# Kernel tuning notes

Hardware: AMD Instinct MI355X
Metric: run time of the kernel (lower is better)

Reference implementation:

```python
import jax, jax.numpy as jnp
import numpy as np

RADIUS = 0.5
HEADS = 4
LATENT = 128
KIN = 3 + 3 + 3 + 1  # q_pos + o_pos + rel + dist
LN_EPS = 1e-5


def setup_inputs() -> dict:
    key = jax.random.key(0)
    ks = jax.random.split(key, 12)
    B, Nq, No = 2, 1024, 1024
    h_obs = jax.random.normal(ks[0], (B, No, LATENT), dtype=jnp.float32)
    pos_obs = jax.random.uniform(ks[1], (B, No, 3), dtype=jnp.float32)
    pos_query = jax.random.uniform(ks[2], (B, Nq, 3), dtype=jnp.float32)
    obs_mask = jax.random.randint(ks[3], (B, No), 0, 2, dtype=jnp.int32)
    # kernel MLP params: Linear(KIN, LATENT) -> ReLU -> Linear(LATENT, HEADS)
    W1 = jax.random.normal(ks[4], (KIN, LATENT), dtype=jnp.float32) * (1.0 / np.sqrt(KIN))
    b1 = jax.random.normal(ks[5], (LATENT,), dtype=jnp.float32) * 0.01
    W2 = jax.random.normal(ks[6], (LATENT, HEADS), dtype=jnp.float32) * (1.0 / np.sqrt(LATENT))
    b2 = jax.random.normal(ks[7], (HEADS,), dtype=jnp.float32) * 0.01
    ln_g = jnp.ones((LATENT,), dtype=jnp.float32)
    ln_b = jnp.zeros((LATENT,), dtype=jnp.float32)
    Wv = jax.random.normal(ks[8], (LATENT, LATENT), dtype=jnp.float32) * (1.0 / np.sqrt(LATENT))
    bv = jax.random.normal(ks[9], (LATENT,), dtype=jnp.float32) * 0.01
    return {"h_obs": h_obs, "pos_obs": pos_obs, "pos_query": pos_query,
            "obs_mask": obs_mask, "W1": W1, "b1": b1, "W2": W2, "b2": b2,
            "ln_g": ln_g, "ln_b": ln_b, "Wv": Wv, "bv": bv}


def reference(h_obs, pos_obs, pos_query, obs_mask, W1, b1, W2, b2, ln_g, ln_b, Wv, bv):
    B, Nq, _ = pos_query.shape
    _, No, _ = pos_obs.shape
    H, D = HEADS, LATENT // HEADS

    # pairwise geometric encoding: (B, Nq, No, *)
    rel = pos_query[:, :, None, :] - pos_obs[:, None, :, :]
    dist = jnp.linalg.norm(rel, axis=-1, keepdims=True)
    q_exp = jnp.broadcast_to(pos_query[:, :, None, :], rel.shape)
    o_exp = jnp.broadcast_to(pos_obs[:, None, :, :], rel.shape)
    kin = jnp.concatenate([q_exp, o_exp, rel, dist], axis=-1)  # (B,Nq,No,KIN)

    # per-pair MLP -> per-head attention logits
    hid = jax.nn.relu(kin @ W1 + b1)                 # (B,Nq,No,LATENT)
    logits = hid @ W2 + b2                           # (B,Nq,No,H)
    logits = jnp.transpose(logits, (0, 3, 1, 2))     # (B,H,Nq,No)

    # radius + observation masking
    neg = jnp.float32(-jnp.inf)
    mask = (dist[..., 0] > RADIUS)[:, None, :, :] | (obs_mask == 0)[:, None, None, :]
    logits = jnp.where(mask, neg, logits)
    weights = jax.nn.softmax(logits, axis=-1)        # (B,H,Nq,No)

    # value path: LayerNorm + projection
    mu = jnp.mean(h_obs, axis=-1, keepdims=True)
    var = jnp.var(h_obs, axis=-1, keepdims=True)
    hn = (h_obs - mu) / jnp.sqrt(var + LN_EPS) * ln_g + ln_b
    v = hn @ Wv + bv                                 # (B,No,LATENT)
    v = jnp.transpose(v.reshape(B, No, H, D), (0, 2, 1, 3))  # (B,H,No,D)

    out = jnp.einsum('bhqo,bhod->bhqd', weights, v)  # (B,H,Nq,D)
    out = jnp.transpose(out, (0, 2, 1, 3)).reshape(B, Nq, H * D)
    return out
```

## Files before the change

### kernel.cpp

```cpp
#include <hip/hip_runtime.h>
#include <math.h>
#include <float.h>

#define B_ 2
#define NQ 1024
#define NO 1024
#define LAT 128
#define NHEADS 4
#define RADIUS_ 0.5f
#define LN_EPS_ 1e-5f
#define CAP 256
#define PPAD 264

#define V_BYTES ((size_t)B_ * NO * LAT * 4)

__device__ __forceinline__ float selh(int h, float a, float b, float c, float d) {
  return h == 0 ? a : (h == 1 ? b : (h == 2 ? c : d));
}


__global__ __launch_bounds__(256) void gano_prep_kernel(
    const float* __restrict__ h_obs, const float* __restrict__ ln_g,
    const float* __restrict__ ln_b, const float* __restrict__ Wv,
    const float* __restrict__ bv, const float* __restrict__ W1,
    const float* __restrict__ b1, const float* __restrict__ W2,
    float* __restrict__ v_out,
    float4* __restrict__ A4, float4* __restrict__ CW8, int write_derived)
{
  const int tid = threadIdx.x;
  const int j = tid & 127;
  const int half = tid >> 7;
  const int wave = tid >> 6;
  const int lane = tid & 63;
  const int r0 = blockIdx.x * 4 + half * 2;

  __shared__ float s_redA[2][4];
  __shared__ float s_redB[2][4];
  __shared__ __align__(16) float s_hn[4][LAT];

  const float x0 = h_obs[(size_t)r0 * LAT + j];
  const float x1 = h_obs[(size_t)(r0 + 1) * LAT + j];
  float s0 = x0, s1 = x1;
  #pragma unroll
  for (int off = 32; off >= 1; off >>= 1) {
    s0 += __shfl_down(s0, off);
    s1 += __shfl_down(s1, off);
  }
  if (lane == 0) { s_redA[0][wave] = s0; s_redA[1][wave] = s1; }
  __syncthreads();
  const float mu0 = (s_redA[0][half * 2] + s_redA[0][half * 2 + 1]) * (1.0f / LAT);
  const float mu1 = (s_redA[1][half * 2] + s_redA[1][half * 2 + 1]) * (1.0f / LAT);
  const float d0 = x0 - mu0, d1 = x1 - mu1;
  float q0 = d0 * d0, q1 = d1 * d1;
  #pragma unroll
  for (int off = 32; off >= 1; off >>= 1) {
    q0 += __shfl_down(q0, off);
    q1 += __shfl_down(q1, off);
  }
  if (lane == 0) { s_redB[0][wave] = q0; s_redB[1][wave] = q1; }
  __syncthreads();
  const float var0 = (s_redB[0][half * 2] + s_redB[0][half * 2 + 1]) * (1.0f / LAT);
  const float var1 = (s_redB[1][half * 2] + s_redB[1][half * 2 + 1]) * (1.0f / LAT);
  const float g = ln_g[j], be = ln_b[j];
  s_hn[half * 2 + 0][j] = d0 * rsqrtf(var0 + LN_EPS_) * g + be;
  s_hn[half * 2 + 1][j] = d1 * rsqrtf(var1 + LN_EPS_) * g + be;
  __syncthreads();

  float a0 = 0.0f, a1 = 0.0f;
  const float4* h0 = (const float4*)s_hn[half * 2 + 0];
  const float4* h1 = (const float4*)s_hn[half * 2 + 1];
  #pragma unroll 4
  for (int k4 = 0; k4 < LAT / 4; ++k4) {
    const float4 u0 = h0[k4];
    const float4 u1 = h1[k4];
    const float w0 = Wv[(k4 * 4 + 0) * LAT + j];
    const float w1 = Wv[(k4 * 4 + 1) * LAT + j];
    const float w2 = Wv[(k4 * 4 + 2) * LAT + j];
    const float w3 = Wv[(k4 * 4 + 3) * LAT + j];
    a0 = fmaf(u0.x, w0, a0); a0 = fmaf(u0.y, w1, a0);
    a0 = fmaf(u0.z, w2, a0); a0 = fmaf(u0.w, w3, a0);
    a1 = fmaf(u1.x, w0, a1); a1 = fmaf(u1.y, w1, a1);
    a1 = fmaf(u1.z, w2, a1); a1 = fmaf(u1.w, w3, a1);
  }
  const float bvj = bv[j];
  v_out[(size_t)(r0 + 0) * LAT + j] = a0 + bvj;
  v_out[(size_t)(r0 + 1) * LAT + j] = a1 + bvj;

  if (write_derived && blockIdx.x == 0 && tid < LAT) {
    float w[10];
    #pragma unroll
    for (int k = 0; k < 10; ++k) w[k] = W1[k * LAT + tid];
    A4[tid] = make_float4(w[0] + w[6], w[1] + w[7], w[2] + w[8], b1[tid]);
    CW8[2 * tid + 0] = make_float4(w[3] - w[6], w[4] - w[7], w[5] - w[8], w[9]);
    CW8[2 * tid + 1] = make_float4(W2[tid * NHEADS + 0], W2[tid * NHEADS + 1],
                                   W2[tid * NHEADS + 2], W2[tid * NHEADS + 3]);
  }
}

template <int NS, bool DERIVED>
__device__ __forceinline__ void flash_pass(
    int lane, int cnt,
    const float4* __restrict__ s_list_w, const int* __restrict__ s_idx_w,
    const float* __restrict__ s_Qw, float* __restrict__ s_pw,
    const float4* __restrict__ CW8,
    const float* __restrict__ W1, const float* __restrict__ W2,
    float b20, float b21, float b22, float b23,
    const float* __restrict__ vb, int hh,
    float& m0, float& m1, float& m2, float& m3,
    float& z0, float& z1, float& z2, float& z3,
    float& ax, float& ay)
{
  float4 C[NS];
  bool act[NS];
  #pragma unroll
  for (int r = 0; r < NS; ++r) {
    const int s = r * 64 + lane;
    act[r] = s < cnt;
    C[r] = s_list_w[act[r] ? s : (cnt - 1)];
  }
  float L[NS][NHEADS];
  #pragma unroll
  for (int r = 0; r < NS; ++r) {
    L[r][0] = b20; L[r][1] = b21; L[r][2] = b22; L[r][3] = b23;
  }

  #pragma unroll 2
  for (int j4 = 0; j4 < LAT / 4; ++j4) {
    const float4 q4 = *(const float4*)&s_Qw[j4 << 2];
    #pragma unroll
    for (int u = 0; u < 4; ++u) {
      const int j = (j4 << 2) + u;
      float4 cw, w2;
      if constexpr (DERIVED) {
        cw = CW8[2 * j + 0];
        w2 = CW8[2 * j + 1];
      } else {
        cw = make_float4(W1[3 * LAT + j] - W1[6 * LAT + j],
                         W1[4 * LAT + j] - W1[7 * LAT + j],
                         W1[5 * LAT + j] - W1[8 * LAT + j],
                         W1[9 * LAT + j]);
        w2 = *(const float4*)&W2[j * NHEADS];
      }
      const float qj = (u == 0) ? q4.x : (u == 1) ? q4.y : (u == 2) ? q4.z : q4.w;
      #pragma unroll
      for (int r = 0; r < NS; ++r) {
        float gg = fmaf(cw.x, C[r].x, qj);
        gg = fmaf(cw.y, C[r].y, gg);
        gg = fmaf(cw.z, C[r].z, gg);
        gg = fmaf(cw.w, C[r].w, gg);
        gg = fmaxf(gg, 0.0f);
        L[r][0] = fmaf(gg, w2.x, L[r][0]);
        L[r][1] = fmaf(gg, w2.y, L[r][1]);
        L[r][2] = fmaf(gg, w2.z, L[r][2]);
        L[r][3] = fmaf(gg, w2.w, L[r][3]);
      }
    }
  }
  #pragma unroll
  for (int r = 0; r < NS; ++r)
    if (!act[r]) { L[r][0] = L[r][1] = L[r][2] = L[r][3] = -FLT_MAX; }

  float x0 = L[0][0], x1 = L[0][1], x2 = L[0][2], x3 = L[0][3];
  #pragma unroll
  for (int r = 1; r < NS; ++r) {
    x0 = fmaxf(x0, L[r][0]); x1 = fmaxf(x1, L[r][1]);
    x2 = fmaxf(x2, L[r][2]); x3 = fmaxf(x3, L[r][3]);
  }
  #pragma unroll
  for (int off = 1; off < 64; off <<= 1) {
    x0 = fmaxf(x0, __shfl_xor(x0, off));
    x1 = fmaxf(x1, __shfl_xor(x1, off));
    x2 = fmaxf(x2, __shfl_xor(x2, off));
    x3 = fmaxf(x3, __shfl_xor(x3, off));
  }
  const float nm0 = fmaxf(m0, x0), nm1 = fmaxf(m1, x1);
  const float nm2 = fmaxf(m2, x2), nm3 = fmaxf(m3, x3);
  const float sc0 = __expf(m0 - nm0), sc1 = __expf(m1 - nm1);
  const float sc2 = __expf(m2 - nm2), sc3 = __expf(m3 - nm3);
  m0 = nm0; m1 = nm1; m2 = nm2; m3 = nm3;

  float pz0 = 0.f, pz1 = 0.f, pz2 = 0.f, pz3 = 0.f;
  #pragma unroll
  for (int r = 0; r < NS; ++r) {
    const float p0 = __expf(L[r][0] - nm0);
    const float p1 = __expf(L[r][1] - nm1);
    const float p2 = __expf(L[r][2] - nm2);
    const float p3 = __expf(L[r][3] - nm3);
    const int s = r * 64 + lane;
    s_pw[0 * PPAD + s] = p0;
    s_pw[1 * PPAD + s] = p1;
    s_pw[2 * PPAD + s] = p2;
    s_pw[3 * PPAD + s] = p3;
    pz0 += p0; pz1 += p1; pz2 += p2; pz3 += p3;
  }
  #pragma unroll
  for (int off = 1; off < 64; off <<= 1) {
    pz0 += __shfl_xor(pz0, off);
    pz1 += __shfl_xor(pz1, off);
    pz2 += __shfl_xor(pz2, off);
    pz3 += __shfl_xor(pz3, off);
  }
  z0 = z0 * sc0 + pz0;
  z1 = z1 * sc1 + pz1;
  z2 = z2 * sc2 + pz2;
  z3 = z3 * sc3 + pz3;

  const float sch = selh(hh, sc0, sc1, sc2, sc3);
  ax *= sch; ay *= sch;
  const float* pr = s_pw + hh * PPAD;
  #pragma unroll 2
  for (int it = 0; it < cnt; it += 4) {
    const float4 pq = *(const float4*)&pr[it];
    const int4 iq = *(const int4*)&s_idx_w[it];
    const float2 v0 = *(const float2*)(vb + (size_t)(iq.x & (NO - 1)) * LAT);
    const float2 v1 = *(const float2*)(vb + (size_t)(iq.y & (NO - 1)) * LAT);
    const float2 v2 = *(const float2*)(vb + (size_t)(iq.z & (NO - 1)) * LAT);
    const float2 v3 = *(const float2*)(vb + (size_t)(iq.w & (NO - 1)) * LAT);
    ax = fmaf(pq.x, v0.x, ax); ay = fmaf(pq.x, v0.y, ay);
    ax = fmaf(pq.y, v1.x, ax); ay = fmaf(pq.y, v1.y, ay);
    ax = fmaf(pq.z, v2.x, ax); ay = fmaf(pq.z, v2.y, ay);
    ax = fmaf(pq.w, v3.x, ax); ay = fmaf(pq.w, v3.y, ay);
  }
}

template <bool DERIVED>
__global__ __launch_bounds__(256, 4) void gano_main_kernel(
    const float* __restrict__ pos_obs, const float* __restrict__ pos_query,
    const int* __restrict__ obs_mask,
    const float* __restrict__ W1, const float* __restrict__ b1,
    const float* __restrict__ W2, const float* __restrict__ b2,
    const float* __restrict__ v,
    const float4* __restrict__ A4, const float4* __restrict__ CW8,
    float* __restrict__ out)
{
  __shared__ __align__(16) float4 s_list[4][CAP];
  __shared__ int   s_idx[4][CAP];
  __shared__ __align__(16) float s_p[4][NHEADS * PPAD];
  __shared__ __align__(16) float s_Q[4][LAT];

  const int tid = threadIdx.x;
  const int wave = tid >> 6, lane = tid & 63;
  const int qg = blockIdx.x * 4 + wave;
  const int b = qg >> 10, q = qg & (NQ - 1);

  const float qx = pos_query[(size_t)qg * 3 + 0];
  const float qy = pos_query[(size_t)qg * 3 + 1];
  const float qz = pos_query[(size_t)qg * 3 + 2];

  #pragma unroll
  for (int jj = lane; jj < LAT; jj += 64) {
    float4 a;
    if constexpr (DERIVED) {
      a = A4[jj];
    } else {
      a = make_float4(W1[0 * LAT + jj] + W1[6 * LAT + jj],
                      W1[1 * LAT + jj] + W1[7 * LAT + jj],
                      W1[2 * LAT + jj] + W1[8 * LAT + jj],
                      b1[jj]);
    }
    s_Q[wave][jj] = fmaf(qx, a.x, fmaf(qy, a.y, fmaf(qz, a.z, a.w)));
  }

  const float* pob = pos_obs + (size_t)b * NO * 3;
  const int*   om  = obs_mask + (size_t)b * NO;
  const float b20 = b2[0], b21 = b2[1], b22 = b2[2], b23 = b2[3];
  const int c0 = lane << 1;
  const int hh = lane >> 4;
  const float* vb = v + (size_t)b * NO * LAT + c0;

  float m0 = -FLT_MAX, m1 = -FLT_MAX, m2 = -FLT_MAX, m3 = -FLT_MAX;
  float z0 = 0.f, z1 = 0.f, z2 = 0.f, z3 = 0.f;
  float ax = 0.f, ay = 0.f;

  const float4* listw = s_list[wave];
  const int*    idxw  = s_idx[wave];
  const float*  Qw    = s_Q[wave];
  float*        pw    = s_p[wave];

  int base = 0, nvtot = 0;

  #define RUN_PASS(N_)                                                        \
    flash_pass<N_, DERIVED>(lane, base, listw, idxw, Qw, pw, CW8, W1, W2,     \
                            b20, b21, b22, b23, vb, hh,                        \
                            m0, m1, m2, m3, z0, z1, z2, z3, ax, ay)
  #define DISPATCH_PASS()                                                     \
    do {                                                                      \
      const int ns_ = (base + 63) >> 6;                                       \
      if (ns_ == 4)      RUN_PASS(4);                                         \
      else if (ns_ == 3) RUN_PASS(3);                                         \
      else if (ns_ == 2) RUN_PASS(2);                                         \
      else               RUN_PASS(1);                                         \
    } while (0)

  for (int rd = 0; rd < 16; ++rd) {
    const int o = (rd << 6) + lane;
    const float ox = pob[o * 3 + 0], oy = pob[o * 3 + 1], oz = pob[o * 3 + 2];
    const float rx = qx - ox, ry = qy - oy, rz = qz - oz;
    const float dist = sqrtf(rx * rx + ry * ry + rz * rz);
    const int ok = (om[o] != 0) && (dist <= RADIUS_);
    const unsigned long long bal = __ballot(ok);
    const int cnt = __popcll(bal);
    if (base + cnt > CAP) {
      DISPATCH_PASS();
      base = 0;
    }
    if (ok) {
      const int pos = base + __popcll(bal & ((1ull << lane) - 1ull));
      s_list[wave][pos] = make_float4(ox, oy, oz, dist);
      s_idx[wave][pos] = o;
    }
    base += cnt;
    nvtot += cnt;
  }
  if (base > 0) DISPATCH_PASS();
  #undef RUN_PASS
  #undef DISPATCH_PASS

  const float zz = selh(hh, z0, z1, z2, z3);
  float2 o2;
  o2.x = (nvtot > 0) ? (ax / zz) : 0.0f;
  o2.y = (nvtot > 0) ? (ay / zz) : 0.0f;
  *(float2*)&out[(size_t)qg * LAT + c0] = o2;
}

extern "C" void kernel_launch(void* const* d_in, const int* in_sizes, int n_in,
                              void* d_out, int out_size, void* d_ws, size_t ws_size,
                              hipStream_t stream) {
  const float* h_obs     = (const float*)d_in[0];
  const float* pos_obs   = (const float*)d_in[1];
  const float* pos_query = (const float*)d_in[2];
  const int*   obs_mask  = (const int*)d_in[3];
  const float* W1        = (const float*)d_in[4];
  const float* b1        = (const float*)d_in[5];
  const float* W2        = (const float*)d_in[6];
  const float* b2        = (const float*)d_in[7];
  const float* ln_g      = (const float*)d_in[8];
  const float* ln_b      = (const float*)d_in[9];
  const float* Wv        = (const float*)d_in[10];
  const float* bv        = (const float*)d_in[11];
  float* outp = (float*)d_out;
  float* v    = (float*)d_ws;

  const size_t need = V_BYTES + 3 * LAT * sizeof(float4);
  const int derived = (ws_size >= need) ? 1 : 0;
  float4* A4  = (float4*)((char*)d_ws + V_BYTES);
  float4* CW8 = A4 + LAT;
  if (!derived) { A4 = (float4*)d_ws; CW8 = (float4*)d_ws; }

  gano_prep_kernel<<<(B_ * NO) / 4, 256, 0, stream>>>(h_obs, ln_g, ln_b, Wv, bv,
                                                      W1, b1, W2, v, A4, CW8, derived);
  if (derived) {
    gano_main_kernel<true><<<(B_ * NQ) / 4, 256, 0, stream>>>(
        pos_obs, pos_query, obs_mask, W1, b1, W2, b2, v,
        (const float4*)A4, (const float4*)CW8, outp);
  } else {
    gano_main_kernel<false><<<(B_ * NQ) / 4, 256, 0, stream>>>(
        pos_obs, pos_query, obs_mask, W1, b1, W2, b2, v,
        (const float4*)A4, (const float4*)CW8, outp);
  }
}
```

Baseline: 44.59 us.

## Split observation range across wave pairs and broadcast MLP weights via readlane

Each query is now handled by two waves, each scanning half of the observations, and the two partial softmax states are merged through shared memory at the end. The grid doubles to twice as many blocks. Per-hidden-unit MLP weights and the query projection are held in registers across lanes and broadcast with readlane, replacing the per-iteration loads from global memory and LDS. This removes the derived-weight precompute from the prep kernel but adds a block barrier and a cross-wave merge step.

```diff
diff --git a/kernel.cpp b/kernel.cpp
--- a/kernel.cpp
+++ b/kernel.cpp
@@ -1,6 +1,7 @@
 #include <hip/hip_runtime.h>
 #include <math.h>
 #include <float.h>
+#include <utility>
 
 #define B_ 2
 #define NQ 1024
@@ -12,20 +13,17 @@
 #define CAP 256
 #define PPAD 264
 
-#define V_BYTES ((size_t)B_ * NO * LAT * 4)
-
 __device__ __forceinline__ float selh(int h, float a, float b, float c, float d) {
   return h == 0 ? a : (h == 1 ? b : (h == 2 ? c : d));
 }
-
+__device__ __forceinline__ float rdlane(float v, int l) {
+  return __int_as_float(__builtin_amdgcn_readlane(__float_as_int(v), l));
+}
 
 __global__ __launch_bounds__(256) void gano_prep_kernel(
     const float* __restrict__ h_obs, const float* __restrict__ ln_g,
     const float* __restrict__ ln_b, const float* __restrict__ Wv,
-    const float* __restrict__ bv, const float* __restrict__ W1,
-    const float* __restrict__ b1, const float* __restrict__ W2,
-    float* __restrict__ v_out,
-    float4* __restrict__ A4, float4* __restrict__ CW8, int write_derived)
+    const float* __restrict__ bv, float* __restrict__ v_out)
 {
   const int tid = threadIdx.x;
   const int j = tid & 127;
@@ -85,180 +83,55 @@
   const float bvj = bv[j];
   v_out[(size_t)(r0 + 0) * LAT + j] = a0 + bvj;
   v_out[(size_t)(r0 + 1) * LAT + j] = a1 + bvj;
-
-  if (write_derived && blockIdx.x == 0 && tid < LAT) {
-    float w[10];
-    #pragma unroll
-    for (int k = 0; k < 10; ++k) w[k] = W1[k * LAT + tid];
-    A4[tid] = make_float4(w[0] + w[6], w[1] + w[7], w[2] + w[8], b1[tid]);
-    CW8[2 * tid + 0] = make_float4(w[3] - w[6], w[4] - w[7], w[5] - w[8], w[9]);
-    CW8[2 * tid + 1] = make_float4(W2[tid * NHEADS + 0], W2[tid * NHEADS + 1],
-                                   W2[tid * NHEADS + 2], W2[tid * NHEADS + 3]);
-  }
-}
-
-template <int NS, bool DERIVED>
-__device__ __forceinline__ void flash_pass(
-    int lane, int cnt,
-    const float4* __restrict__ s_list_w, const int* __restrict__ s_idx_w,
-    const float* __restrict__ s_Qw, float* __restrict__ s_pw,
-    const float4* __restrict__ CW8,
-    const float* __restrict__ W1, const float* __restrict__ W2,
-    float b20, float b21, float b22, float b23,
-    const float* __restrict__ vb, int hh,
-    float& m0, float& m1, float& m2, float& m3,
-    float& z0, float& z1, float& z2, float& z3,
-    float& ax, float& ay)
-{
-  float4 C[NS];
-  bool act[NS];
-  #pragma unroll
-  for (int r = 0; r < NS; ++r) {
-    const int s = r * 64 + lane;
-    act[r] = s < cnt;
-    C[r] = s_list_w[act[r] ? s : (cnt - 1)];
-  }
-  float L[NS][NHEADS];
-  #pragma unroll
-  for (int r = 0; r < NS; ++r) {
-    L[r][0] = b20; L[r][1] = b21; L[r][2] = b22; L[r][3] = b23;
-  }
-
-  #pragma unroll 2
-  for (int j4 = 0; j4 < LAT / 4; ++j4) {
-    const float4 q4 = *(const float4*)&s_Qw[j4 << 2];
-    #pragma unroll
-    for (int u = 0; u < 4; ++u) {
-      const int j = (j4 << 2) + u;
-      float4 cw, w2;
-      if constexpr (DERIVED) {
-        cw = CW8[2 * j + 0];
-        w2 = CW8[2 * j + 1];
-      } else {
-        cw = make_float4(W1[3 * LAT + j] - W1[6 * LAT + j],
-                         W1[4 * LAT + j] - W1[7 * LAT + j],
-                         W1[5 * LAT + j] - W1[8 * LAT + j],
-                         W1[9 * LAT + j]);
-        w2 = *(const float4*)&W2[j * NHEADS];
-      }
-      const float qj = (u == 0) ? q4.x : (u == 1) ? q4.y : (u == 2) ? q4.z : q4.w;
-      #pragma unroll
-      for (int r = 0; r < NS; ++r) {
-        float gg = fmaf(cw.x, C[r].x, qj);
-        gg = fmaf(cw.y, C[r].y, gg);
-        gg = fmaf(cw.z, C[r].z, gg);
-        gg = fmaf(cw.w, C[r].w, gg);
-        gg = fmaxf(gg, 0.0f);
-        L[r][0] = fmaf(gg, w2.x, L[r][0]);
-        L[r][1] = fmaf(gg, w2.y, L[r][1]);
-        L[r][2] = fmaf(gg, w2.z, L[r][2]);
-        L[r][3] = fmaf(gg, w2.w, L[r][3]);
-      }
-    }
-  }
-  #pragma unroll
-  for (int r = 0; r < NS; ++r)
-    if (!act[r]) { L[r][0] = L[r][1] = L[r][2] = L[r][3] = -FLT_MAX; }
-
-  float x0 = L[0][0], x1 = L[0][1], x2 = L[0][2], x3 = L[0][3];
-  #pragma unroll
-  for (int r = 1; r < NS; ++r) {
-    x0 = fmaxf(x0, L[r][0]); x1 = fmaxf(x1, L[r][1]);
-    x2 = fmaxf(x2, L[r][2]); x3 = fmaxf(x3, L[r][3]);
-  }
-  #pragma unroll
-  for (int off = 1; off < 64; off <<= 1) {
-    x0 = fmaxf(x0, __shfl_xor(x0, off));
-    x1 = fmaxf(x1, __shfl_xor(x1, off));
-    x2 = fmaxf(x2, __shfl_xor(x2, off));
-    x3 = fmaxf(x3, __shfl_xor(x3, off));
-  }
-  const float nm0 = fmaxf(m0, x0), nm1 = fmaxf(m1, x1);
-  const float nm2 = fmaxf(m2, x2), nm3 = fmaxf(m3, x3);
-  const float sc0 = __expf(m0 - nm0), sc1 = __expf(m1 - nm1);
-  const float sc2 = __expf(m2 - nm2), sc3 = __expf(m3 - nm3);
-  m0 = nm0; m1 = nm1; m2 = nm2; m3 = nm3;
-
-  float pz0 = 0.f, pz1 = 0.f, pz2 = 0.f, pz3 = 0.f;
-  #pragma unroll
-  for (int r = 0; r < NS; ++r) {
-    const float p0 = __expf(L[r][0] - nm0);
-    const float p1 = __expf(L[r][1] - nm1);
-    const float p2 = __expf(L[r][2] - nm2);
-    const float p3 = __expf(L[r][3] - nm3);
-    const int s = r * 64 + lane;
-    s_pw[0 * PPAD + s] = p0;
-    s_pw[1 * PPAD + s] = p1;
-    s_pw[2 * PPAD + s] = p2;
-    s_pw[3 * PPAD + s] = p3;
-    pz0 += p0; pz1 += p1; pz2 += p2; pz3 += p3;
-  }
-  #pragma unroll
-  for (int off = 1; off < 64; off <<= 1) {
-    pz0 += __shfl_xor(pz0, off);
-    pz1 += __shfl_xor(pz1, off);
-    pz2 += __shfl_xor(pz2, off);
-    pz3 += __shfl_xor(pz3, off);
-  }
-  z0 = z0 * sc0 + pz0;
-  z1 = z1 * sc1 + pz1;
-  z2 = z2 * sc2 + pz2;
-  z3 = z3 * sc3 + pz3;
-
-  const float sch = selh(hh, sc0, sc1, sc2, sc3);
-  ax *= sch; ay *= sch;
-  const float* pr = s_pw + hh * PPAD;
-  #pragma unroll 2
-  for (int it = 0; it < cnt; it += 4) {
-    const float4 pq = *(const float4*)&pr[it];
-    const int4 iq = *(const int4*)&s_idx_w[it];
-    const float2 v0 = *(const float2*)(vb + (size_t)(iq.x & (NO - 1)) * LAT);
-    const float2 v1 = *(const float2*)(vb + (size_t)(iq.y & (NO - 1)) * LAT);
-    const float2 v2 = *(const float2*)(vb + (size_t)(iq.z & (NO - 1)) * LAT);
-    const float2 v3 = *(const float2*)(vb + (size_t)(iq.w & (NO - 1)) * LAT);
-    ax = fmaf(pq.x, v0.x, ax); ay = fmaf(pq.x, v0.y, ay);
-    ax = fmaf(pq.y, v1.x, ax); ay = fmaf(pq.y, v1.y, ay);
-    ax = fmaf(pq.z, v2.x, ax); ay = fmaf(pq.z, v2.y, ay);
-    ax = fmaf(pq.w, v3.x, ax); ay = fmaf(pq.w, v3.y, ay);
-  }
-}
-
-template <bool DERIVED>
+}
+
 __global__ __launch_bounds__(256, 4) void gano_main_kernel(
     const float* __restrict__ pos_obs, const float* __restrict__ pos_query,
     const int* __restrict__ obs_mask,
     const float* __restrict__ W1, const float* __restrict__ b1,
     const float* __restrict__ W2, const float* __restrict__ b2,
-    const float* __restrict__ v,
-    const float4* __restrict__ A4, const float4* __restrict__ CW8,
-    float* __restrict__ out)
+    const float* __restrict__ v, float* __restrict__ out)
 {
   __shared__ __align__(16) float4 s_list[4][CAP];
   __shared__ int   s_idx[4][CAP];
   __shared__ __align__(16) float s_p[4][NHEADS * PPAD];
-  __shared__ __align__(16) float s_Q[4][LAT];
+  __shared__ __align__(16) float s_acc[4][LAT];
+  __shared__ float s_mz[4][2][NHEADS];
+  __shared__ int   s_cnt4[4];
 
   const int tid = threadIdx.x;
   const int wave = tid >> 6, lane = tid & 63;
-  const int qg = blockIdx.x * 4 + wave;
-  const int b = qg >> 10, q = qg & (NQ - 1);
+  const int qg = blockIdx.x * 2 + (wave >> 1);
+  const int hhalf = wave & 1;
+  const int b = qg >> 10;
 
   const float qx = pos_query[(size_t)qg * 3 + 0];
   const float qy = pos_query[(size_t)qg * 3 + 1];
   const float qz = pos_query[(size_t)qg * 3 + 2];
 
-  #pragma unroll
-  for (int jj = lane; jj < LAT; jj += 64) {
-    float4 a;
-    if constexpr (DERIVED) {
-      a = A4[jj];
-    } else {
-      a = make_float4(W1[0 * LAT + jj] + W1[6 * LAT + jj],
-                      W1[1 * LAT + jj] + W1[7 * LAT + jj],
-                      W1[2 * LAT + jj] + W1[8 * LAT + jj],
-                      b1[jj]);
-    }
-    s_Q[wave][jj] = fmaf(qx, a.x, fmaf(qy, a.y, fmaf(qz, a.z, a.w)));
+  float wA0, wA1, wA2, wA3, wA4, wA5, wA6, wA7, qA;
+  float wB0, wB1, wB2, wB3, wB4, wB5, wB6, wB7, qB;
+  {
+    const int jj = lane;
+    const float r0 = W1[0 * LAT + jj], r1 = W1[1 * LAT + jj], r2 = W1[2 * LAT + jj];
+    const float r3 = W1[3 * LAT + jj], r4 = W1[4 * LAT + jj], r5 = W1[5 * LAT + jj];
+    const float r6 = W1[6 * LAT + jj], r7 = W1[7 * LAT + jj], r8 = W1[8 * LAT + jj];
+    const float r9 = W1[9 * LAT + jj];
+    wA0 = r3 - r6; wA1 = r4 - r7; wA2 = r5 - r8; wA3 = r9;
+    const float4 w2r = *(const float4*)&W2[jj * NHEADS];
+    wA4 = w2r.x; wA5 = w2r.y; wA6 = w2r.z; wA7 = w2r.w;
+    qA = b1[jj] + qx * (r0 + r6) + qy * (r1 + r7) + qz * (r2 + r8);
+  }
+  {
+    const int jj = 64 + lane;
+    const float r0 = W1[0 * LAT + jj], r1 = W1[1 * LAT + jj], r2 = W1[2 * LAT + jj];
+    const float r3 = W1[3 * LAT + jj], r4 = W1[4 * LAT + jj], r5 = W1[5 * LAT + jj];
+    const float r6 = W1[6 * LAT + jj], r7 = W1[7 * LAT + jj], r8 = W1[8 * LAT + jj];
+    const float r9 = W1[9 * LAT + jj];
+    wB0 = r3 - r6; wB1 = r4 - r7; wB2 = r5 - r8; wB3 = r9;
+    const float4 w2r = *(const float4*)&W2[jj * NHEADS];
+    wB4 = w2r.x; wB5 = w2r.y; wB6 = w2r.z; wB7 = w2r.w;
+    qB = b1[jj] + qx * (r0 + r6) + qy * (r1 + r7) + qz * (r2 + r8);
   }
 
   const float* pob = pos_obs + (size_t)b * NO * 3;
@@ -272,55 +145,173 @@
   float z0 = 0.f, z1 = 0.f, z2 = 0.f, z3 = 0.f;
   float ax = 0.f, ay = 0.f;
 
-  const float4* listw = s_list[wave];
-  const int*    idxw  = s_idx[wave];
-  const float*  Qw    = s_Q[wave];
-  float*        pw    = s_p[wave];
-
+  float4* listw = s_list[wave];
+  int*    idxw  = s_idx[wave];
+  float*  pw    = s_p[wave];
   int base = 0, nvtot = 0;
 
-  #define RUN_PASS(N_)                                                        \
-    flash_pass<N_, DERIVED>(lane, base, listw, idxw, Qw, pw, CW8, W1, W2,     \
-                            b20, b21, b22, b23, vb, hh,                        \
-                            m0, m1, m2, m3, z0, z1, z2, z3, ax, ay)
-  #define DISPATCH_PASS()                                                     \
-    do {                                                                      \
-      const int ns_ = (base + 63) >> 6;                                       \
-      if (ns_ == 4)      RUN_PASS(4);                                         \
-      else if (ns_ == 3) RUN_PASS(3);                                         \
-      else if (ns_ == 2) RUN_PASS(2);                                         \
-      else               RUN_PASS(1);                                         \
-    } while (0)
-
-  for (int rd = 0; rd < 16; ++rd) {
-    const int o = (rd << 6) + lane;
+  auto flash = [&](auto nsc) {
+    constexpr int NS = decltype(nsc)::value;
+    const int cnt = base;
+    float4 C[NS];
+    bool act[NS];
+    #pragma unroll
+    for (int r = 0; r < NS; ++r) {
+      const int s = r * 64 + lane;
+      act[r] = s < cnt;
+      C[r] = listw[act[r] ? s : (cnt - 1)];
+    }
+    float L[NS][NHEADS];
+    #pragma unroll
+    for (int r = 0; r < NS; ++r) {
+      L[r][0] = b20; L[r][1] = b21; L[r][2] = b22; L[r][3] = b23;
+    }
+
+    auto half_loop = [&](float hw0, float hw1, float hw2, float hw3,
+                         float hw4, float hw5, float hw6, float hw7, float hq) {
+      #pragma unroll 4
+      for (int l = 0; l < 64; ++l) {
+        const float qj = rdlane(hq, l);
+        const float cw0 = rdlane(hw0, l), cw1 = rdlane(hw1, l);
+        const float cw2 = rdlane(hw2, l), cw3 = rdlane(hw3, l);
+        const float u0 = rdlane(hw4, l), u1 = rdlane(hw5, l);
+        const float u2 = rdlane(hw6, l), u3 = rdlane(hw7, l);
+        #pragma unroll
+        for (int r = 0; r < NS; ++r) {
+          float gg = fmaf(cw0, C[r].x, qj);
+          gg = fmaf(cw1, C[r].y, gg);
+          gg = fmaf(cw2, C[r].z, gg);
+          gg = fmaf(cw3, C[r].w, gg);
+          gg = fmaxf(gg, 0.0f);
+          L[r][0] = fmaf(gg, u0, L[r][0]);
+          L[r][1] = fmaf(gg, u1, L[r][1]);
+          L[r][2] = fmaf(gg, u2, L[r][2]);
+          L[r][3] = fmaf(gg, u3, L[r][3]);
+        }
+      }
+    };
+    half_loop(wA0, wA1, wA2, wA3, wA4, wA5, wA6, wA7, qA);
+    half_loop(wB0, wB1, wB2, wB3, wB4, wB5, wB6, wB7, qB);
+
+    #pragma unroll
+    for (int r = 0; r < NS; ++r)
+      if (!act[r]) { L[r][0] = L[r][1] = L[r][2] = L[r][3] = -FLT_MAX; }
+
+    float x0 = L[0][0], x1 = L[0][1], x2 = L[0][2], x3 = L[0][3];
+    #pragma unroll
+    for (int r = 1; r < NS; ++r) {
+      x0 = fmaxf(x0, L[r][0]); x1 = fmaxf(x1, L[r][1]);
+      x2 = fmaxf(x2, L[r][2]); x3 = fmaxf(x3, L[r][3]);
+    }
+    #pragma unroll
+    for (int off = 1; off < 64; off <<= 1) {
+      x0 = fmaxf(x0, __shfl_xor(x0, off));
+      x1 = fmaxf(x1, __shfl_xor(x1, off));
+      x2 = fmaxf(x2, __shfl_xor(x2, off));
+      x3 = fmaxf(x3, __shfl_xor(x3, off));
+    }
+    const float nm0 = fmaxf(m0, x0), nm1 = fmaxf(m1, x1);
+    const float nm2 = fmaxf(m2, x2), nm3 = fmaxf(m3, x3);
+    const float sc0 = __expf(m0 - nm0), sc1 = __expf(m1 - nm1);
+    const float sc2 = __expf(m2 - nm2), sc3 = __expf(m3 - nm3);
+    m0 = nm0; m1 = nm1; m2 = nm2; m3 = nm3;
+
+    float pz0 = 0.f, pz1 = 0.f, pz2 = 0.f, pz3 = 0.f;
+    #pragma unroll
+    for (int r = 0; r < NS; ++r) {
+      const float p0 = __expf(L[r][0] - nm0);
+      const float p1 = __expf(L[r][1] - nm1);
+      const float p2 = __expf(L[r][2] - nm2);
+      const float p3 = __expf(L[r][3] - nm3);
+      const int s = r * 64 + lane;
+      pw[0 * PPAD + s] = p0;
+      pw[1 * PPAD + s] = p1;
+      pw[2 * PPAD + s] = p2;
+      pw[3 * PPAD + s] = p3;
+      pz0 += p0; pz1 += p1; pz2 += p2; pz3 += p3;
+    }
+    #pragma unroll
+    for (int off = 1; off < 64; off <<= 1) {
+      pz0 += __shfl_xor(pz0, off);
+      pz1 += __shfl_xor(pz1, off);
+      pz2 += __shfl_xor(pz2, off);
+      pz3 += __shfl_xor(pz3, off);
+    }
+    z0 = z0 * sc0 + pz0;
+    z1 = z1 * sc1 + pz1;
+    z2 = z2 * sc2 + pz2;
+    z3 = z3 * sc3 + pz3;
+
+    const float sch = selh(hh, sc0, sc1, sc2, sc3);
+    ax *= sch; ay *= sch;
+    const float* pr = pw + hh * PPAD;
+    #pragma unroll 2
+    for (int it = 0; it < cnt; it += 4) {
+      const float4 pq = *(const float4*)&pr[it];
+      const int4 iq = *(const int4*)&idxw[it];
+      const float2 v0 = *(const float2*)(vb + (size_t)(iq.x & (NO - 1)) * LAT);
+      const float2 v1 = *(const float2*)(vb + (size_t)(iq.y & (NO - 1)) * LAT);
+      const float2 v2 = *(const float2*)(vb + (size_t)(iq.z & (NO - 1)) * LAT);
+      const float2 v3 = *(const float2*)(vb + (size_t)(iq.w & (NO - 1)) * LAT);
+      ax = fmaf(pq.x, v0.x, ax); ay = fmaf(pq.x, v0.y, ay);
+      ax = fmaf(pq.y, v1.x, ax); ay = fmaf(pq.y, v1.y, ay);
+      ax = fmaf(pq.z, v2.x, ax); ay = fmaf(pq.z, v2.y, ay);
+      ax = fmaf(pq.w, v3.x, ax); ay = fmaf(pq.w, v3.y, ay);
+    }
+  };
+  auto dispatch = [&]() {
+    const int ns = (base + 63) >> 6;
+    if (ns == 4)      flash(std::integral_constant<int, 4>{});
+    else if (ns == 3) flash(std::integral_constant<int, 3>{});
+    else if (ns == 2) flash(std::integral_constant<int, 2>{});
+    else              flash(std::integral_constant<int, 1>{});
+  };
+
+  for (int rd = 0; rd < 8; ++rd) {
+    const int o = (hhalf << 9) + (rd << 6) + lane;
     const float ox = pob[o * 3 + 0], oy = pob[o * 3 + 1], oz = pob[o * 3 + 2];
     const float rx = qx - ox, ry = qy - oy, rz = qz - oz;
     const float dist = sqrtf(rx * rx + ry * ry + rz * rz);
     const int ok = (om[o] != 0) && (dist <= RADIUS_);
     const unsigned long long bal = __ballot(ok);
     const int cnt = __popcll(bal);
-    if (base + cnt > CAP) {
-      DISPATCH_PASS();
-      base = 0;
-    }
+    if (base + cnt > CAP) { dispatch(); base = 0; }
     if (ok) {
       const int pos = base + __popcll(bal & ((1ull << lane) - 1ull));
-      s_list[wave][pos] = make_float4(ox, oy, oz, dist);
-      s_idx[wave][pos] = o;
+      listw[pos] = make_float4(ox, oy, oz, dist);
+      idxw[pos] = o;
     }
     base += cnt;
     nvtot += cnt;
   }
-  if (base > 0) DISPATCH_PASS();
-  #undef RUN_PASS
-  #undef DISPATCH_PASS
-
-  const float zz = selh(hh, z0, z1, z2, z3);
-  float2 o2;
-  o2.x = (nvtot > 0) ? (ax / zz) : 0.0f;
-  o2.y = (nvtot > 0) ? (ay / zz) : 0.0f;
-  *(float2*)&out[(size_t)qg * LAT + c0] = o2;
+  if (base > 0) dispatch();
+
+  if (lane == 0) {
+    s_mz[wave][0][0] = m0; s_mz[wave][0][1] = m1;
+    s_mz[wave][0][2] = m2; s_mz[wave][0][3] = m3;
+    s_mz[wave][1][0] = z0; s_mz[wave][1][1] = z1;
+    s_mz[wave][1][2] = z2; s_mz[wave][1][3] = z3;
+    s_cnt4[wave] = nvtot;
+  }
+  s_acc[wave][c0] = ax;
+  s_acc[wave][c0 + 1] = ay;
+  __syncthreads();
+
+  {
+    const int pair = tid >> 7;
+    const int col = tid & 127;
+    const int wA = pair * 2, wB = wA + 1;
+    const int h = col >> 5;
+    const int qout = blockIdx.x * 2 + pair;
+    const int ct = s_cnt4[wA] + s_cnt4[wB];
+    const float mA = s_mz[wA][0][h], mB = s_mz[wB][0][h];
+    const float M = fmaxf(mA, mB);
+    const float eA = __expf(mA - M), eB = __expf(mB - M);
+    const float num = eA * s_acc[wA][col] + eB * s_acc[wB][col];
+    const float den = eA * s_mz[wA][1][h] + eB * s_mz[wB][1][h];
+    const float r = (ct > 0) ? (num / den) : 0.0f;
+    out[(size_t)qout * LAT + col] = r;
+  }
 }
 
 extern "C" void kernel_launch(void* const* d_in, const int* in_sizes, int n_in,
@@ -341,21 +332,7 @@
   float* outp = (float*)d_out;
   float* v    = (float*)d_ws;
 
-  const size_t need = V_BYTES + 3 * LAT * sizeof(float4);
-  const int derived = (ws_size >= need) ? 1 : 0;
-  float4* A4  = (float4*)((char*)d_ws + V_BYTES);
-  float4* CW8 = A4 + LAT;
-  if (!derived) { A4 = (float4*)d_ws; CW8 = (float4*)d_ws; }
-
-  gano_prep_kernel<<<(B_ * NO) / 4, 256, 0, stream>>>(h_obs, ln_g, ln_b, Wv, bv,
-                                                      W1, b1, W2, v, A4, CW8, derived);
-  if (derived) {
-    gano_main_kernel<true><<<(B_ * NQ) / 4, 256, 0, stream>>>(
-        pos_obs, pos_query, obs_mask, W1, b1, W2, b2, v,
-        (const float4*)A4, (const float4*)CW8, outp);
-  } else {
-    gano_main_kernel<false><<<(B_ * NQ) / 4, 256, 0, stream>>>(
-        pos_obs, pos_query, obs_mask, W1, b1, W2, b2, v,
-        (const float4*)A4, (const float4*)CW8, outp);
-  }
-}
+  gano_prep_kernel<<<(B_ * NO) / 4, 256, 0, stream>>>(h_obs, ln_g, ln_b, Wv, bv, v);
+  gano_main_kernel<<<B_ * NQ / 2, 256, 0, stream>>>(pos_obs, pos_query, obs_mask,
+                                                    W1, b1, W2, b2, v, outp);
+}
```

Measured after the change: 117.4 us. 2.63x slower.
